# Optimization experiments

Hardware: AMD Instinct MI355X
Metric: run time of the kernel (lower is better)

Reference implementation:

```python
import jax, jax.numpy as jnp
import numpy as np
from jax import lax

B, S, H, T = 64, 512, 1024, 48


def setup_inputs() -> dict:
    key = jax.random.key(0)
    ks = jax.random.split(key, 8)
    x = jax.random.normal(ks[0], (B, S, H), dtype=jnp.float32)
    # left-aligned variable-length attention mask (lengths in [S//2, S])
    lengths = jax.random.randint(ks[1], (B,), S // 2, S + 1)
    attention_mask = (jnp.arange(S)[None, :] < lengths[:, None]).astype(jnp.int32)
    labels = jax.random.randint(ks[2], (B, S), 0, T).astype(jnp.int64)
    # decoder Linear(H, T)
    W = jax.random.normal(ks[3], (H, T), dtype=jnp.float32) / np.sqrt(H)
    b = jnp.zeros((T,), dtype=jnp.float32)
    # CRF parameters (allennlp-style: transitions + start/end transitions)
    transitions = jax.random.normal(ks[4], (T, T), dtype=jnp.float32) * 0.1
    start_trans = jax.random.normal(ks[5], (T,), dtype=jnp.float32) * 0.1
    end_trans = jax.random.normal(ks[6], (T,), dtype=jnp.float32) * 0.1
    return {"x": x, "attention_mask": attention_mask, "labels": labels,
            "W": W, "b": b, "transitions": transitions,
            "start_trans": start_trans, "end_trans": end_trans}


def _log_partition(logits, mask, trans, start, end):
    # logits [B,S,T], mask [B,S] int. Returns logZ [B].
    alpha0 = start[None, :] + logits[:, 0]                     # [B,T]
    emits = jnp.moveaxis(logits[:, 1:], 1, 0)                  # [S-1,B,T]
    ms = mask[:, 1:].T                                         # [S-1,B]

    def step(alpha, inp):
        emit, m = inp
        inner = alpha[:, :, None] + trans[None, :, :] + emit[:, None, :]  # [B,T,T]
        new = jax.nn.logsumexp(inner, axis=1)
        alpha = jnp.where(m[:, None] > 0, new, alpha)
        return alpha, None

    alpha, _ = lax.scan(step, alpha0, (emits, ms))
    return jax.nn.logsumexp(alpha + end[None, :], axis=1)      # [B]


def _gold_score(logits, labels, mask, trans, start, end):
    maskf = mask.astype(logits.dtype)
    emit = jnp.take_along_axis(logits, labels[..., None], axis=2)[..., 0]  # [B,S]
    emit_score = jnp.sum(emit * maskf, axis=1)
    tr = trans[labels[:, :-1], labels[:, 1:]]                   # [B,S-1]
    trans_score = jnp.sum(tr * maskf[:, 1:], axis=1)
    last_idx = jnp.sum(mask, axis=1) - 1                        # [B]
    last_tags = jnp.take_along_axis(labels, last_idx[:, None], axis=1)[:, 0]
    return start[labels[:, 0]] + emit_score + trans_score + end[last_tags]


def _viterbi(logits, mask, trans, start, end):
    Bn, Sn, Tn = logits.shape
    v0 = start[None, :] + logits[:, 0]
    emits = jnp.moveaxis(logits[:, 1:], 1, 0)                  # [S-1,B,T]
    ms = mask[:, 1:].T
    ident = jnp.broadcast_to(jnp.arange(Tn, dtype=jnp.int32)[None, :], (Bn, Tn))

    def step(v, inp):
        emit, m = inp
        scores = v[:, :, None] + trans[None, :, :]              # [B,T_prev,T_cur]
        bp = jnp.argmax(scores, axis=1).astype(jnp.int32)       # [B,T]
        best = jnp.max(scores, axis=1) + emit
        v_new = jnp.where(m[:, None] > 0, best, v)
        bp = jnp.where(m[:, None] > 0, bp, ident)               # identity at padded steps
        return v_new, bp

    v, bps = lax.scan(step, v0, (emits, ms))                    # bps [S-1,B,T]
    last = jnp.argmax(v + end[None, :], axis=1).astype(jnp.int32)  # [B]

    def back(tag, bp):
        prev = jnp.take_along_axis(bp, tag[:, None], axis=1)[:, 0]
        return prev, tag

    first_tag, rest = lax.scan(back, last, bps, reverse=True)   # rest [S-1,B]
    tags = jnp.concatenate([first_tag[:, None], rest.T], axis=1)  # [B,S]
    return (tags * mask).astype(jnp.int64)                      # pad with zeros


def reference(x, attention_mask, labels, W, b, transitions, start_trans, end_trans):
    features = jnp.einsum('bsh,ht->bst', x, W) + b              # decoder Linear
    pred_labels = _viterbi(features, attention_mask, transitions, start_trans, end_trans)
    logZ = _log_partition(features, attention_mask, transitions, start_trans, end_trans)
    gold = _gold_score(features, labels, attention_mask, transitions, start_trans, end_trans)
    loss = -jnp.sum(gold - logZ)                                # -log-likelihood, summed over batch
    return features, pred_labels, loss
```

## Files before the change

### kernel.cpp

```cpp
#include <hip/hip_runtime.h>
#include <hip/hip_bf16.h>
#include <math.h>

#define Bn 64
#define Sn 512
#define Hn 1024
#define Tn 48

#define LOG2E 1.4426950408889634f
#define LN2f  0.6931471805599453f

#define PRED_OFF (Bn*Sn*Tn)
#define LOSS_OFF (PRED_OFF + Bn*Sn)

#define RL(x,i) __int_as_float(__builtin_amdgcn_readlane(__float_as_int(x),(i)))

#if __has_builtin(__builtin_amdgcn_exp2f)
#define EXP2(x) __builtin_amdgcn_exp2f(x)
#else
#define EXP2(x) exp2f(x)
#endif
#if __has_builtin(__builtin_amdgcn_logf)
#define LOG2(x) __builtin_amdgcn_logf(x)
#else
#define LOG2(x) log2f(x)
#endif

__device__ __forceinline__ unsigned umin2(unsigned a, unsigned b) { return a < b ? a : b; }

#define DOT4(ACC,A,B) { ACC = fmaf((A).x,(B).x,ACC); ACC = fmaf((A).y,(B).y,ACC); ACC = fmaf((A).z,(B).z,ACC); ACC = fmaf((A).w,(B).w,ACC); }

__global__ __launch_bounds__(256) void gemm_feat(
    const float* __restrict__ x, const float* __restrict__ W,
    const float* __restrict__ bias, float* __restrict__ feat)
{
  __shared__ __align__(16) float xs[64][68];
  __shared__ __align__(16) float wsT[Tn][68];
  const int tid = threadIdx.x;
  const int srow = tid >> 2;
  const int sqc  = tid & 3;
  const int ty = tid >> 3;
  const int tx = tid & 7;
  const size_t row0 = (size_t)blockIdx.x * 64;

  float4 xreg[4];
  float  wreg[12];
  #pragma unroll
  for (int p = 0; p < 4; ++p)
    xreg[p] = *reinterpret_cast<const float4*>(&x[(row0 + srow)*Hn + (sqc + p*4)*4]);
  #pragma unroll
  for (int i = 0; i < 12; ++i) {
    const int id = tid + i*256; const int kk = id/Tn; const int t = id - kk*Tn;
    wreg[i] = W[(size_t)kk*Tn + t];
  }

  float acc[2][6];
  #pragma unroll
  for (int r = 0; r < 2; ++r)
    #pragma unroll
    for (int c = 0; c < 6; ++c) acc[r][c] = 0.f;

  for (int k0 = 0; k0 < Hn; k0 += 64) {
    #pragma unroll
    for (int p = 0; p < 4; ++p)
      *reinterpret_cast<float4*>(&xs[srow][(sqc + p*4)*4]) = xreg[p];
    #pragma unroll
    for (int i = 0; i < 12; ++i) {
      const int id = tid + i*256; const int kk = id/Tn; const int t = id - kk*Tn;
      wsT[t][kk] = wreg[i];
    }
    __syncthreads();
    if (k0 + 64 < Hn) {
      #pragma unroll
      for (int p = 0; p < 4; ++p)
        xreg[p] = *reinterpret_cast<const float4*>(&x[(row0 + srow)*Hn + (k0+64) + (sqc + p*4)*4]);
      #pragma unroll
      for (int i = 0; i < 12; ++i) {
        const int id = tid + i*256; const int kk = id/Tn; const int t = id - kk*Tn;
        wreg[i] = W[(size_t)(k0 + 64 + kk)*Tn + t];
      }
    }
    #pragma unroll 4
    for (int kk = 0; kk < 64; kk += 4) {
      const float4 a0 = *reinterpret_cast<const float4*>(&xs[ty*2+0][kk]);
      const float4 a1 = *reinterpret_cast<const float4*>(&xs[ty*2+1][kk]);
      const float4 w0 = *reinterpret_cast<const float4*>(&wsT[tx*6+0][kk]);
      const float4 w1 = *reinterpret_cast<const float4*>(&wsT[tx*6+1][kk]);
      const float4 w2 = *reinterpret_cast<const float4*>(&wsT[tx*6+2][kk]);
      const float4 w3 = *reinterpret_cast<const float4*>(&wsT[tx*6+3][kk]);
      const float4 w4 = *reinterpret_cast<const float4*>(&wsT[tx*6+4][kk]);
      const float4 w5 = *reinterpret_cast<const float4*>(&wsT[tx*6+5][kk]);
      DOT4(acc[0][0],a0,w0) DOT4(acc[0][1],a0,w1) DOT4(acc[0][2],a0,w2)
      DOT4(acc[0][3],a0,w3) DOT4(acc[0][4],a0,w4) DOT4(acc[0][5],a0,w5)
      DOT4(acc[1][0],a1,w0) DOT4(acc[1][1],a1,w1) DOT4(acc[1][2],a1,w2)
      DOT4(acc[1][3],a1,w3) DOT4(acc[1][4],a1,w4) DOT4(acc[1][5],a1,w5)
    }
    __syncthreads();
  }
  #pragma unroll
  for (int c = 0; c < 6; ++c) {
    const int col = tx*6 + c;
    const float bv = bias[col];
    #pragma unroll
    for (int r = 0; r < 2; ++r)
      feat[(row0 + ty*2 + r)*Tn + col] = acc[r][c] + bv;
  }
}

__global__ __launch_bounds__(64, 1) void crf_kernel(
    const float* __restrict__ feat,
    const int* __restrict__ mask,
    const int* __restrict__ labels,
    const float* __restrict__ trans,
    const float* __restrict__ startv,
    const float* __restrict__ endv,
    float* __restrict__ pred_out,
    float* __restrict__ wsLogZ,
    float* __restrict__ wsGold)
{
  __shared__ unsigned char bpL[Sn * 64];
  __shared__ unsigned char pathL[384 * 64];
  __shared__ __align__(16) float slds[64];
  __shared__ int EA[8];

  const int role = blockIdx.x >> 6;
  const int b    = blockIdx.x & 63;
  const int lane = threadIdx.x;
  const float* fb = feat + (size_t)b * Sn * Tn;

  int lc = 0;
  #pragma unroll
  for (int it = 0; it < Sn/64; ++it) lc += (mask[(size_t)b*Sn + it*64 + lane] != 0);
  #pragma unroll
  for (int off = 32; off; off >>= 1) lc += __shfl_xor(lc, off);
  const int len = lc;

  const int j = (lane < Tn) ? lane : (Tn - 1);
  const float4* sv4 = reinterpret_cast<const float4*>(slds);

  if (role == 0) {
    float Ev[48];
    #pragma unroll
    for (int i = 0; i < 48; ++i) Ev[i] = EXP2(trans[i*Tn + j] * LOG2E);
    const float a0 = (startv[j] + fb[j]) * LOG2E;
    float Zref = RL(a0, 0);
    float beta = a0 - Zref;
    slds[lane] = EXP2(beta);
    float em2 = fb[Tn + j] * LOG2E;
    for (int t = 1; t < len; ++t) {
      const int tn = (t + 1 < len) ? (t + 1) : t;
      const float em_nxt = fb[(size_t)tn*Tn + j] * LOG2E;
      float4 av[12];
      #pragma unroll
      for (int k = 0; k < 12; ++k) av[k] = sv4[k];
      float s0=0.f, s1=0.f, s2=0.f, s3=0.f;
      #pragma unroll
      for (int k = 0; k < 12; ++k) {
        s0 = fmaf(av[k].x, Ev[4*k+0], s0);
        s1 = fmaf(av[k].y, Ev[4*k+1], s1);
        s2 = fmaf(av[k].z, Ev[4*k+2], s2);
        s3 = fmaf(av[k].w, Ev[4*k+3], s3);
      }
      const float dj = LOG2((s0 + s1) + (s2 + s3)) + em2;
      const float d0 = RL(dj, 0);
      Zref += d0;
      const float nb = dj - d0;
      slds[lane] = EXP2(nb);
      beta = nb;
      em2 = em_nxt;
    }
    float fv = (lane < Tn) ? beta + endv[lane] * LOG2E : -INFINITY;
    float m = fv;
    #pragma unroll
    for (int off = 32; off; off >>= 1) m = fmaxf(m, __shfl_xor(m, off));
    float e = (lane < Tn) ? EXP2(fv - m) : 0.f;
    #pragma unroll
    for (int off = 32; off; off >>= 1) e += __shfl_xor(e, off);
    if (lane == 0) wsLogZ[b] = (Zref + m + LOG2(e)) * LN2f;

  } else if (role == 1) {
    float trv[48];
    #pragma unroll
    for (int i = 0; i < 48; ++i) trv[i] = trans[i*Tn + j];
    float v = startv[j] + fb[j];
    slds[lane] = v;
    float em_cur = fb[Tn + j];
    for (int t = 1; t < len; ++t) {
      const int tn = (t + 1 < len) ? (t + 1) : t;
      const float em_nxt = fb[(size_t)tn*Tn + j];
      float4 av[12];
      #pragma unroll
      for (int k = 0; k < 12; ++k) av[k] = sv4[k];
      float q[48];
      #pragma unroll
      for (int k = 0; k < 12; ++k) {
        q[4*k+0] = av[k].x + trv[4*k+0];
        q[4*k+1] = av[k].y + trv[4*k+1];
        q[4*k+2] = av[k].z + trv[4*k+2];
        q[4*k+3] = av[k].w + trv[4*k+3];
      }
      float m16[16];
      #pragma unroll
      for (int u = 0; u < 16; ++u)
        m16[u] = fmaxf(fmaxf(q[3*u], q[3*u+1]), q[3*u+2]);
      float m6a = fmaxf(fmaxf(m16[0],  m16[1]),  m16[2]);
      float m6b = fmaxf(fmaxf(m16[3],  m16[4]),  m16[5]);
      float m6c = fmaxf(fmaxf(m16[6],  m16[7]),  m16[8]);
      float m6d = fmaxf(fmaxf(m16[9],  m16[10]), m16[11]);
      float m6e = fmaxf(fmaxf(m16[12], m16[13]), m16[14]);
      float m6f = m16[15];
      const float best = fmaxf(fmaxf(fmaxf(m6a,m6b),m6c),
                               fmaxf(fmaxf(m6d,m6e),m6f));
      unsigned s16[16];
      #pragma unroll
      for (int u = 0; u < 16; ++u) {
        const unsigned ka = __float_as_uint(q[3*u]   - best) | (unsigned)(3*u);
        const unsigned kb = __float_as_uint(q[3*u+1] - best) | (unsigned)(3*u+1);
        const unsigned kc = __float_as_uint(q[3*u+2] - best) | (unsigned)(3*u+2);
        s16[u] = umin2(umin2(ka, kb), kc);
      }
      unsigned i6a = umin2(umin2(s16[0],  s16[1]),  s16[2]);
      unsigned i6b = umin2(umin2(s16[3],  s16[4]),  s16[5]);
      unsigned i6c = umin2(umin2(s16[6],  s16[7]),  s16[8]);
      unsigned i6d = umin2(umin2(s16[9],  s16[10]), s16[11]);
      unsigned i6e = umin2(umin2(s16[12], s16[13]), s16[14]);
      unsigned i6f = s16[15];
      const unsigned bidx = umin2(umin2(umin2(i6a,i6b),i6c), umin2(umin2(i6d,i6e),i6f));
      bpL[t*64 + lane] = (unsigned char)bidx;
      v = best + em_cur;
      slds[lane] = v;
      em_cur = em_nxt;
    }
    for (int t = len; t < Sn; ++t) bpL[t*64 + lane] = (unsigned char)lane;

    float fv = (lane < Tn) ? v + endv[lane] : -INFINITY;
    int fi = (lane < Tn) ? lane : 64;
    #pragma unroll
    for (int off = 32; off; off >>= 1) {
      const float ov = __shfl_xor(fv, off);
      const int   oi = __shfl_xor(fi, off);
      if (ov > fv || (ov == fv && oi < fi)) { fv = ov; fi = oi; }
    }
    __syncthreads();

    #define JOB(r) \
      const int id##r  = lane + 64*(r); \
      const int seg##r = id##r & 7;     \
      int cur##r = id##r >> 3;          \
      const int bpb##r = seg##r << 12;  \
      const int pb##r  = id##r << 6;    \
      pathL[pb##r + 63] = (unsigned char)cur##r;
    JOB(0) JOB(1) JOB(2) JOB(3) JOB(4) JOB(5)
    for (int d = 62; d >= 0; --d) {
      const int o = (d + 1) << 6;
      cur0 = bpL[bpb0 + o + cur0]; pathL[pb0 + d] = (unsigned char)cur0;
      cur1 = bpL[bpb1 + o + cur1]; pathL[pb1 + d] = (unsigned char)cur1;
      cur2 = bpL[bpb2 + o + cur2]; pathL[pb2 + d] = (unsigned char)cur2;
      cur3 = bpL[bpb3 + o + cur3]; pathL[pb3 + d] = (unsigned char)cur3;
      cur4 = bpL[bpb4 + o + cur4]; pathL[pb4 + d] = (unsigned char)cur4;
      cur5 = bpL[bpb5 + o + cur5]; pathL[pb5 + d] = (unsigned char)cur5;
    }
    #undef JOB
    __syncthreads();
    if (lane == 0) {
      int Ecur = fi;
      EA[7] = Ecur;
      for (int s = 7; s >= 1; --s) {
        const int bottom = pathL[((Ecur << 3) + s) * 64];
        Ecur = bpL[(s << 12) + bottom];
        EA[s-1] = Ecur;
      }
    }
    __syncthreads();
    #pragma unroll
    for (int r8 = 0; r8 < 8; ++r8) {
      const int t = r8*64 + lane;
      const int pv = pathL[((EA[r8] << 3) + r8) * 64 + lane];
      pred_out[(size_t)b*Sn + t] = (t < len) ? (float)pv : 0.f;
    }

  } else {
    float g = 0.f;
    #pragma unroll
    for (int it = 0; it < Sn/64; ++it) {
      const int sg = it*64 + lane;
      if (sg < len) {
        const int la = labels[(size_t)b*Sn + sg];
        float e = fb[(size_t)sg*Tn + la];
        if (sg > 0) e += trans[labels[(size_t)b*Sn + sg - 1]*Tn + la];
        g += e;
      }
    }
    #pragma unroll
    for (int off = 32; off; off >>= 1) g += __shfl_xor(g, off);
    if (lane == 0) {
      g += startv[labels[(size_t)b*Sn]] + endv[labels[(size_t)b*Sn + len - 1]];
      wsGold[b] = g;
    }
  }
}

__global__ void loss_reduce(const float* __restrict__ wsLogZ,
                            const float* __restrict__ wsGold,
                            float* __restrict__ out)
{
  const int lane = threadIdx.x;
  float v = wsLogZ[lane] - wsGold[lane];
  #pragma unroll
  for (int off = 32; off; off >>= 1) v += __shfl_xor(v, off);
  if (lane == 0) out[0] = v;
}

extern "C" void kernel_launch(void* const* d_in, const int* in_sizes, int n_in,
                              void* d_out, int out_size, void* d_ws, size_t ws_size,
                              hipStream_t stream) {
  const float* x      = (const float*)d_in[0];
  const int*   mask   = (const int*)  d_in[1];
  const int*   labels = (const int*)  d_in[2];
  const float* W      = (const float*)d_in[3];
  const float* bias   = (const float*)d_in[4];
  const float* trans  = (const float*)d_in[5];
  const float* startv = (const float*)d_in[6];
  const float* endv   = (const float*)d_in[7];

  float* out  = (float*)d_out;
  float* feat = out;
  float* pred = out + PRED_OFF;
  float* loss = out + LOSS_OFF;
  float* wsLogZ = (float*)d_ws;
  float* wsGold = wsLogZ + 64;

  gemm_feat<<<(Bn*Sn)/64, 256, 0, stream>>>(x, W, bias, feat);
  crf_kernel<<<192, 64, 0, stream>>>(feat, mask, labels, trans, startv, endv, pred, wsLogZ, wsGold);
  loss_reduce<<<1, 64, 0, stream>>>(wsLogZ, wsGold, loss);
}
```

Baseline: 323.9 us.

## Split Viterbi into serial max-scan, parallel backpointer pass, and backtrace kernel

```diff
diff --git a/kernel.cpp b/kernel.cpp
--- a/kernel.cpp
+++ b/kernel.cpp
@@ -27,6 +27,10 @@
 #endif
 
 __device__ __forceinline__ unsigned umin2(unsigned a, unsigned b) { return a < b ? a : b; }
+
+#define VWS_BYTE_OFF 512
+#define BPW_BYTE_OFF (512 + (size_t)Bn*Sn*Tn*4)
+#define WS_NEED (BPW_BYTE_OFF + (size_t)Bn*Sn*Tn)
 
 #define DOT4(ACC,A,B) { ACC = fmaf((A).x,(B).x,ACC); ACC = fmaf((A).y,(B).y,ACC); ACC = fmaf((A).z,(B).z,ACC); ACC = fmaf((A).w,(B).w,ACC); }
 
@@ -107,7 +111,284 @@
   }
 }
 
-__global__ __launch_bounds__(64, 1) void crf_kernel(
+__device__ __forceinline__ int seq_len(const int* __restrict__ mask, int b, int lane) {
+  int lc = 0;
+  #pragma unroll
+  for (int it = 0; it < Sn/64; ++it) lc += (mask[(size_t)b*Sn + it*64 + lane] != 0);
+  #pragma unroll
+  for (int off = 32; off; off >>= 1) lc += __shfl_xor(lc, off);
+  return lc;
+}
+
+__global__ __launch_bounds__(64, 1) void crf_scan(
+    const float* __restrict__ feat,
+    const int* __restrict__ mask,
+    const int* __restrict__ labels,
+    const float* __restrict__ trans,
+    const float* __restrict__ startv,
+    const float* __restrict__ endv,
+    float* __restrict__ vws,
+    float* __restrict__ wsLogZ,
+    float* __restrict__ wsGold)
+{
+  const int role = blockIdx.x >> 6;
+  const int b    = blockIdx.x & 63;
+  const int lane = threadIdx.x;
+  const float* fb = feat + (size_t)b * Sn * Tn;
+  const int len = seq_len(mask, b, lane);
+  const int j = (lane < Tn) ? lane : (Tn - 1);
+
+  if (role == 0) {
+    float Ev[48];
+    #pragma unroll
+    for (int i = 0; i < 48; ++i) Ev[i] = EXP2(trans[i*Tn + j] * LOG2E);
+    float emq[8];
+    #pragma unroll
+    for (int d = 0; d < 8; ++d) {
+      int s = 1 + d; s = s < len ? s : len - 1;
+      emq[d] = fb[(size_t)s * Tn + j];
+    }
+    const float a0 = (startv[j] + fb[j]) * LOG2E;
+    float Zref = RL(a0, 0);
+    float beta = a0 - Zref;
+    float p = EXP2(beta);
+    for (int t = 1; t < len; t += 8) {
+      #pragma unroll
+      for (int u = 0; u < 8; ++u) {
+        const int tt = t + u;
+        if (tt < len) {
+          const float em2 = emq[u] * LOG2E;
+          int tf = tt + 8; tf = tf < len ? tf : len - 1;
+          emq[u] = fb[(size_t)tf * Tn + j];
+          float s0=0.f, s1=0.f, s2=0.f, s3=0.f;
+          #pragma unroll
+          for (int k = 0; k < 12; ++k) {
+            s0 = fmaf(RL(p, 4*k+0), Ev[4*k+0], s0);
+            s1 = fmaf(RL(p, 4*k+1), Ev[4*k+1], s1);
+            s2 = fmaf(RL(p, 4*k+2), Ev[4*k+2], s2);
+            s3 = fmaf(RL(p, 4*k+3), Ev[4*k+3], s3);
+          }
+          const float dj = LOG2((s0 + s1) + (s2 + s3)) + em2;
+          const float d0 = RL(dj, 0);
+          Zref += d0;
+          beta = dj - d0;
+          p = EXP2(beta);
+        }
+      }
+    }
+    float fv = (lane < Tn) ? beta + endv[lane] * LOG2E : -INFINITY;
+    float m = fv;
+    #pragma unroll
+    for (int off = 32; off; off >>= 1) m = fmaxf(m, __shfl_xor(m, off));
+    float e = (lane < Tn) ? EXP2(fv - m) : 0.f;
+    #pragma unroll
+    for (int off = 32; off; off >>= 1) e += __shfl_xor(e, off);
+    if (lane == 0) wsLogZ[b] = (Zref + m + LOG2(e)) * LN2f;
+
+  } else if (role == 1) {
+    float trv[48];
+    #pragma unroll
+    for (int i = 0; i < 48; ++i) trv[i] = trans[i*Tn + j];
+    float emq[8];
+    #pragma unroll
+    for (int d = 0; d < 8; ++d) {
+      int s = 1 + d; s = s < len ? s : len - 1;
+      emq[d] = fb[(size_t)s * Tn + j];
+    }
+    float v = startv[j] + fb[j];
+    if (lane < Tn) vws[(size_t)b*Sn*Tn + lane] = v;
+    for (int t = 1; t < len; t += 8) {
+      #pragma unroll
+      for (int u = 0; u < 8; ++u) {
+        const int tt = t + u;
+        if (tt < len) {
+          const float em_cur = emq[u];
+          int tf = tt + 8; tf = tf < len ? tf : len - 1;
+          emq[u] = fb[(size_t)tf * Tn + j];
+          float q[48];
+          #pragma unroll
+          for (int i = 0; i < 48; ++i) q[i] = RL(v, i) + trv[i];
+          float m16[16];
+          #pragma unroll
+          for (int uu = 0; uu < 16; ++uu)
+            m16[uu] = fmaxf(fmaxf(q[3*uu], q[3*uu+1]), q[3*uu+2]);
+          float m6a = fmaxf(fmaxf(m16[0],  m16[1]),  m16[2]);
+          float m6b = fmaxf(fmaxf(m16[3],  m16[4]),  m16[5]);
+          float m6c = fmaxf(fmaxf(m16[6],  m16[7]),  m16[8]);
+          float m6d = fmaxf(fmaxf(m16[9],  m16[10]), m16[11]);
+          float m6e = fmaxf(fmaxf(m16[12], m16[13]), m16[14]);
+          const float best = fmaxf(fmaxf(fmaxf(m6a,m6b),m6c),
+                                   fmaxf(fmaxf(m6d,m6e),m16[15]));
+          v = best + em_cur;
+          if (lane < Tn) vws[((size_t)b*Sn + tt)*Tn + lane] = v;
+        }
+      }
+    }
+
+  } else {
+    float g = 0.f;
+    #pragma unroll
+    for (int it = 0; it < Sn/64; ++it) {
+      const int sg = it*64 + lane;
+      if (sg < len) {
+        const int la = labels[(size_t)b*Sn + sg];
+        float e = fb[(size_t)sg*Tn + la];
+        if (sg > 0) e += trans[labels[(size_t)b*Sn + sg - 1]*Tn + la];
+        g += e;
+      }
+    }
+    #pragma unroll
+    for (int off = 32; off; off >>= 1) g += __shfl_xor(g, off);
+    if (lane == 0) {
+      g += startv[labels[(size_t)b*Sn]] + endv[labels[(size_t)b*Sn + len - 1]];
+      wsGold[b] = g;
+    }
+  }
+}
+
+__global__ __launch_bounds__(256) void bp_kernel(
+    const float* __restrict__ vws,
+    const int* __restrict__ mask,
+    const float* __restrict__ trans,
+    unsigned char* __restrict__ bpw)
+{
+  const int b    = blockIdx.x >> 3;
+  const int oct  = blockIdx.x & 7;
+  const int wv   = threadIdx.x >> 6;
+  const int lane = threadIdx.x & 63;
+  const int len = seq_len(mask, b, lane);
+  const int j = (lane < Tn) ? lane : (Tn - 1);
+
+  float trv[48];
+  #pragma unroll
+  for (int i = 0; i < 48; ++i) trv[i] = trans[i*Tn + j];
+
+  const int t0 = oct*64 + wv*16;
+  #pragma unroll 2
+  for (int i = 0; i < 16; ++i) {
+    const int t = t0 + i;
+    int te = t; te = te < 1 ? 1 : te; te = te < len ? te : len - 1;
+    const float4* vp = reinterpret_cast<const float4*>(vws + ((size_t)b*Sn + te - 1)*Tn);
+    float q[48];
+    #pragma unroll
+    for (int k = 0; k < 12; ++k) {
+      const float4 a = vp[k];
+      q[4*k+0] = a.x + trv[4*k+0];
+      q[4*k+1] = a.y + trv[4*k+1];
+      q[4*k+2] = a.z + trv[4*k+2];
+      q[4*k+3] = a.w + trv[4*k+3];
+    }
+    float m16[16];
+    #pragma unroll
+    for (int u = 0; u < 16; ++u)
+      m16[u] = fmaxf(fmaxf(q[3*u], q[3*u+1]), q[3*u+2]);
+    float m6a = fmaxf(fmaxf(m16[0],  m16[1]),  m16[2]);
+    float m6b = fmaxf(fmaxf(m16[3],  m16[4]),  m16[5]);
+    float m6c = fmaxf(fmaxf(m16[6],  m16[7]),  m16[8]);
+    float m6d = fmaxf(fmaxf(m16[9],  m16[10]), m16[11]);
+    float m6e = fmaxf(fmaxf(m16[12], m16[13]), m16[14]);
+    const float best = fmaxf(fmaxf(fmaxf(m6a,m6b),m6c),
+                             fmaxf(fmaxf(m6d,m6e),m16[15]));
+    unsigned s16[16];
+    #pragma unroll
+    for (int u = 0; u < 16; ++u) {
+      const unsigned ka = __float_as_uint(q[3*u]   - best) | (unsigned)(3*u);
+      const unsigned kb = __float_as_uint(q[3*u+1] - best) | (unsigned)(3*u+1);
+      const unsigned kc = __float_as_uint(q[3*u+2] - best) | (unsigned)(3*u+2);
+      s16[u] = umin2(umin2(ka, kb), kc);
+    }
+    unsigned i6a = umin2(umin2(s16[0],  s16[1]),  s16[2]);
+    unsigned i6b = umin2(umin2(s16[3],  s16[4]),  s16[5]);
+    unsigned i6c = umin2(umin2(s16[6],  s16[7]),  s16[8]);
+    unsigned i6d = umin2(umin2(s16[9],  s16[10]), s16[11]);
+    unsigned i6e = umin2(umin2(s16[12], s16[13]), s16[14]);
+    const unsigned bidx = umin2(umin2(umin2(i6a,i6b),i6c), umin2(umin2(i6d,i6e),s16[15]));
+    if (t >= 1 && t < len && lane < Tn)
+      bpw[((size_t)b*Sn + t)*Tn + lane] = (unsigned char)bidx;
+  }
+}
+
+__device__ __forceinline__ unsigned idw(int a) {
+  return (unsigned)a | ((unsigned)(a+1)<<8) | ((unsigned)(a+2)<<16) | ((unsigned)(a+3)<<24);
+}
+
+__global__ __launch_bounds__(64, 1) void backtrace_kernel(
+    const float* __restrict__ vws,
+    const unsigned char* __restrict__ bpw,
+    const int* __restrict__ mask,
+    const float* __restrict__ endv,
+    float* __restrict__ pred_out)
+{
+  __shared__ unsigned char bpL[Sn * Tn];
+  __shared__ unsigned char pathL[384 * 64];
+  __shared__ int EA[8];
+
+  const int b    = blockIdx.x;
+  const int lane = threadIdx.x;
+  const int len = seq_len(mask, b, lane);
+
+  {
+    const uint4* gb = reinterpret_cast<const uint4*>(bpw + (size_t)b*Sn*Tn);
+    uint4* bl = reinterpret_cast<uint4*>(bpL);
+    for (int i4 = lane; i4 < Sn*Tn/16; i4 += 64) {
+      const int byte0 = i4*16;
+      const int t = byte0 / Tn;
+      const int j0 = byte0 - t*Tn;
+      uint4 val;
+      if (t >= 1 && t < len) val = gb[i4];
+      else { val.x = idw(j0); val.y = idw(j0+4); val.z = idw(j0+8); val.w = idw(j0+12); }
+      bl[i4] = val;
+    }
+  }
+
+  float fv = (lane < Tn) ? vws[((size_t)b*Sn + len - 1)*Tn + lane] + endv[lane] : -INFINITY;
+  int fi = (lane < Tn) ? lane : 64;
+  #pragma unroll
+  for (int off = 32; off; off >>= 1) {
+    const float ov = __shfl_xor(fv, off);
+    const int   oi = __shfl_xor(fi, off);
+    if (ov > fv || (ov == fv && oi < fi)) { fv = ov; fi = oi; }
+  }
+  __syncthreads();
+
+  #define JOB(r) \
+    const int id##r  = lane + 64*(r); \
+    const int seg##r = id##r & 7;     \
+    int cur##r = id##r >> 3;          \
+    const int bpb##r = seg##r * 64 * Tn; \
+    const int pb##r  = id##r << 6;    \
+    pathL[pb##r + 63] = (unsigned char)cur##r;
+  JOB(0) JOB(1) JOB(2) JOB(3) JOB(4) JOB(5)
+  for (int d = 62; d >= 0; --d) {
+    const int o = (d + 1) * Tn;
+    cur0 = bpL[bpb0 + o + cur0]; pathL[pb0 + d] = (unsigned char)cur0;
+    cur1 = bpL[bpb1 + o + cur1]; pathL[pb1 + d] = (unsigned char)cur1;
+    cur2 = bpL[bpb2 + o + cur2]; pathL[pb2 + d] = (unsigned char)cur2;
+    cur3 = bpL[bpb3 + o + cur3]; pathL[pb3 + d] = (unsigned char)cur3;
+    cur4 = bpL[bpb4 + o + cur4]; pathL[pb4 + d] = (unsigned char)cur4;
+    cur5 = bpL[bpb5 + o + cur5]; pathL[pb5 + d] = (unsigned char)cur5;
+  }
+  #undef JOB
+  __syncthreads();
+  if (lane == 0) {
+    int Ecur = fi;
+    EA[7] = Ecur;
+    for (int s = 7; s >= 1; --s) {
+      const int bottom = pathL[((Ecur << 3) + s) * 64];
+      Ecur = bpL[(s * 64) * Tn + bottom];
+      EA[s-1] = Ecur;
+    }
+  }
+  __syncthreads();
+  #pragma unroll
+  for (int r8 = 0; r8 < 8; ++r8) {
+    const int t = r8*64 + lane;
+    const int pv = pathL[((EA[r8] << 3) + r8) * 64 + lane];
+    pred_out[(size_t)b*Sn + t] = (t < len) ? (float)pv : 0.f;
+  }
+}
+
+__global__ __launch_bounds__(64, 1) void crf_kernel_fb(
     const float* __restrict__ feat,
     const int* __restrict__ mask,
     const int* __restrict__ labels,
@@ -127,14 +408,7 @@
   const int b    = blockIdx.x & 63;
   const int lane = threadIdx.x;
   const float* fb = feat + (size_t)b * Sn * Tn;
-
-  int lc = 0;
-  #pragma unroll
-  for (int it = 0; it < Sn/64; ++it) lc += (mask[(size_t)b*Sn + it*64 + lane] != 0);
-  #pragma unroll
-  for (int off = 32; off; off >>= 1) lc += __shfl_xor(lc, off);
-  const int len = lc;
-
+  const int len = seq_len(mask, b, lane);
   const int j = (lane < Tn) ? lane : (Tn - 1);
   const float4* sv4 = reinterpret_cast<const float4*>(slds);
 
@@ -201,38 +475,35 @@
       }
       float m16[16];
       #pragma unroll
-      for (int u = 0; u < 16; ++u)
-        m16[u] = fmaxf(fmaxf(q[3*u], q[3*u+1]), q[3*u+2]);
+      for (int uu = 0; uu < 16; ++uu)
+        m16[uu] = fmaxf(fmaxf(q[3*uu], q[3*uu+1]), q[3*uu+2]);
       float m6a = fmaxf(fmaxf(m16[0],  m16[1]),  m16[2]);
       float m6b = fmaxf(fmaxf(m16[3],  m16[4]),  m16[5]);
       float m6c = fmaxf(fmaxf(m16[6],  m16[7]),  m16[8]);
       float m6d = fmaxf(fmaxf(m16[9],  m16[10]), m16[11]);
       float m6e = fmaxf(fmaxf(m16[12], m16[13]), m16[14]);
-      float m6f = m16[15];
       const float best = fmaxf(fmaxf(fmaxf(m6a,m6b),m6c),
-                               fmaxf(fmaxf(m6d,m6e),m6f));
+                               fmaxf(fmaxf(m6d,m6e),m16[15]));
+      v = best + em_cur;
+      slds[lane] = v;
       unsigned s16[16];
       #pragma unroll
-      for (int u = 0; u < 16; ++u) {
-        const unsigned ka = __float_as_uint(q[3*u]   - best) | (unsigned)(3*u);
-        const unsigned kb = __float_as_uint(q[3*u+1] - best) | (unsigned)(3*u+1);
-        const unsigned kc = __float_as_uint(q[3*u+2] - best) | (unsigned)(3*u+2);
-        s16[u] = umin2(umin2(ka, kb), kc);
+      for (int uu = 0; uu < 16; ++uu) {
+        const unsigned ka = __float_as_uint(q[3*uu]   - best) | (unsigned)(3*uu);
+        const unsigned kb = __float_as_uint(q[3*uu+1] - best) | (unsigned)(3*uu+1);
+        const unsigned kc = __float_as_uint(q[3*uu+2] - best) | (unsigned)(3*uu+2);
+        s16[uu] = umin2(umin2(ka, kb), kc);
       }
       unsigned i6a = umin2(umin2(s16[0],  s16[1]),  s16[2]);
       unsigned i6b = umin2(umin2(s16[3],  s16[4]),  s16[5]);
       unsigned i6c = umin2(umin2(s16[6],  s16[7]),  s16[8]);
       unsigned i6d = umin2(umin2(s16[9],  s16[10]), s16[11]);
       unsigned i6e = umin2(umin2(s16[12], s16[13]), s16[14]);
-      unsigned i6f = s16[15];
-      const unsigned bidx = umin2(umin2(umin2(i6a,i6b),i6c), umin2(umin2(i6d,i6e),i6f));
+      const unsigned bidx = umin2(umin2(umin2(i6a,i6b),i6c), umin2(umin2(i6d,i6e),s16[15]));
       bpL[t*64 + lane] = (unsigned char)bidx;
-      v = best + em_cur;
-      slds[lane] = v;
       em_cur = em_nxt;
     }
     for (int t = len; t < Sn; ++t) bpL[t*64 + lane] = (unsigned char)lane;
-
     float fv = (lane < Tn) ? v + endv[lane] : -INFINITY;
     int fi = (lane < Tn) ? lane : 64;
     #pragma unroll
@@ -242,15 +513,14 @@
       if (ov > fv || (ov == fv && oi < fi)) { fv = ov; fi = oi; }
     }
     __syncthreads();
-
-    #define JOB(r) \
+    #define JOBF(r) \
       const int id##r  = lane + 64*(r); \
       const int seg##r = id##r & 7;     \
       int cur##r = id##r >> 3;          \
       const int bpb##r = seg##r << 12;  \
       const int pb##r  = id##r << 6;    \
       pathL[pb##r + 63] = (unsigned char)cur##r;
-    JOB(0) JOB(1) JOB(2) JOB(3) JOB(4) JOB(5)
+    JOBF(0) JOBF(1) JOBF(2) JOBF(3) JOBF(4) JOBF(5)
     for (int d = 62; d >= 0; --d) {
       const int o = (d + 1) << 6;
       cur0 = bpL[bpb0 + o + cur0]; pathL[pb0 + d] = (unsigned char)cur0;
@@ -260,7 +530,7 @@
       cur4 = bpL[bpb4 + o + cur4]; pathL[pb4 + d] = (unsigned char)cur4;
       cur5 = bpL[bpb5 + o + cur5]; pathL[pb5 + d] = (unsigned char)cur5;
     }
-    #undef JOB
+    #undef JOBF
     __syncthreads();
     if (lane == 0) {
       int Ecur = fi;
@@ -278,7 +548,6 @@
       const int pv = pathL[((EA[r8] << 3) + r8) * 64 + lane];
       pred_out[(size_t)b*Sn + t] = (t < len) ? (float)pv : 0.f;
     }
-
   } else {
     float g = 0.f;
     #pragma unroll
@@ -331,6 +600,15 @@
   float* wsGold = wsLogZ + 64;
 
   gemm_feat<<<(Bn*Sn)/64, 256, 0, stream>>>(x, W, bias, feat);
-  crf_kernel<<<192, 64, 0, stream>>>(feat, mask, labels, trans, startv, endv, pred, wsLogZ, wsGold);
+
+  if (ws_size >= WS_NEED) {
+    float* vws = (float*)((char*)d_ws + VWS_BYTE_OFF);
+    unsigned char* bpw = (unsigned char*)d_ws + BPW_BYTE_OFF;
+    crf_scan<<<192, 64, 0, stream>>>(feat, mask, labels, trans, startv, endv, vws, wsLogZ, wsGold);
+    bp_kernel<<<512, 256, 0, stream>>>(vws, mask, trans, bpw);
+    backtrace_kernel<<<64, 64, 0, stream>>>(vws, bpw, mask, endv, pred);
+  } else {
+    crf_kernel_fb<<<192, 64, 0, stream>>>(feat, mask, labels, trans, startv, endv, pred, wsLogZ, wsGold);
+  }
   loss_reduce<<<1, 64, 0, stream>>>(wsLogZ, wsGold, loss);
 }
```

Result: slower. 366.9 us (+13.3%).

## Move Viterbi backpointer argmax off the serial scan into a parallel kernel

Applied to the files above, without the earlier changes.

```diff
diff --git a/kernel.cpp b/kernel.cpp
--- a/kernel.cpp
+++ b/kernel.cpp
@@ -26,7 +26,12 @@
 #define LOG2(x) log2f(x)
 #endif
 
+#define PIN(x) asm volatile("" : "+v"(x))
+
 __device__ __forceinline__ unsigned umin2(unsigned a, unsigned b) { return a < b ? a : b; }
+
+#define VWS_BYTE_OFF 512
+#define BPW_BYTE_OFF (512 + (size_t)Bn*Sn*Tn*4)
 
 #define DOT4(ACC,A,B) { ACC = fmaf((A).x,(B).x,ACC); ACC = fmaf((A).y,(B).y,ACC); ACC = fmaf((A).z,(B).z,ACC); ACC = fmaf((A).w,(B).w,ACC); }
 
@@ -34,36 +39,36 @@
     const float* __restrict__ x, const float* __restrict__ W,
     const float* __restrict__ bias, float* __restrict__ feat)
 {
-  __shared__ __align__(16) float xs[64][68];
+  __shared__ __align__(16) float xs[128][68];
   __shared__ __align__(16) float wsT[Tn][68];
   const int tid = threadIdx.x;
-  const int srow = tid >> 2;
-  const int sqc  = tid & 3;
+  const int srow  = tid >> 1;
+  const int shalf = tid & 1;
   const int ty = tid >> 3;
   const int tx = tid & 7;
-  const size_t row0 = (size_t)blockIdx.x * 64;
-
-  float4 xreg[4];
+  const size_t row0 = (size_t)blockIdx.x * 128;
+
+  float4 xreg[8];
   float  wreg[12];
   #pragma unroll
-  for (int p = 0; p < 4; ++p)
-    xreg[p] = *reinterpret_cast<const float4*>(&x[(row0 + srow)*Hn + (sqc + p*4)*4]);
+  for (int p = 0; p < 8; ++p)
+    xreg[p] = *reinterpret_cast<const float4*>(&x[(row0 + srow)*Hn + shalf*32 + p*4]);
   #pragma unroll
   for (int i = 0; i < 12; ++i) {
     const int id = tid + i*256; const int kk = id/Tn; const int t = id - kk*Tn;
     wreg[i] = W[(size_t)kk*Tn + t];
   }
 
-  float acc[2][6];
-  #pragma unroll
-  for (int r = 0; r < 2; ++r)
+  float acc[4][6];
+  #pragma unroll
+  for (int r = 0; r < 4; ++r)
     #pragma unroll
     for (int c = 0; c < 6; ++c) acc[r][c] = 0.f;
 
   for (int k0 = 0; k0 < Hn; k0 += 64) {
     #pragma unroll
-    for (int p = 0; p < 4; ++p)
-      *reinterpret_cast<float4*>(&xs[srow][(sqc + p*4)*4]) = xreg[p];
+    for (int p = 0; p < 8; ++p)
+      *reinterpret_cast<float4*>(&xs[srow][shalf*32 + p*4]) = xreg[p];
     #pragma unroll
     for (int i = 0; i < 12; ++i) {
       const int id = tid + i*256; const int kk = id/Tn; const int t = id - kk*Tn;
@@ -72,8 +77,8 @@
     __syncthreads();
     if (k0 + 64 < Hn) {
       #pragma unroll
-      for (int p = 0; p < 4; ++p)
-        xreg[p] = *reinterpret_cast<const float4*>(&x[(row0 + srow)*Hn + (k0+64) + (sqc + p*4)*4]);
+      for (int p = 0; p < 8; ++p)
+        xreg[p] = *reinterpret_cast<const float4*>(&x[(row0 + srow)*Hn + (k0+64) + shalf*32 + p*4]);
       #pragma unroll
       for (int i = 0; i < 12; ++i) {
         const int id = tid + i*256; const int kk = id/Tn; const int t = id - kk*Tn;
@@ -82,8 +87,10 @@
     }
     #pragma unroll 4
     for (int kk = 0; kk < 64; kk += 4) {
-      const float4 a0 = *reinterpret_cast<const float4*>(&xs[ty*2+0][kk]);
-      const float4 a1 = *reinterpret_cast<const float4*>(&xs[ty*2+1][kk]);
+      const float4 a0 = *reinterpret_cast<const float4*>(&xs[ty*4+0][kk]);
+      const float4 a1 = *reinterpret_cast<const float4*>(&xs[ty*4+1][kk]);
+      const float4 a2 = *reinterpret_cast<const float4*>(&xs[ty*4+2][kk]);
+      const float4 a3 = *reinterpret_cast<const float4*>(&xs[ty*4+3][kk]);
       const float4 w0 = *reinterpret_cast<const float4*>(&wsT[tx*6+0][kk]);
       const float4 w1 = *reinterpret_cast<const float4*>(&wsT[tx*6+1][kk]);
       const float4 w2 = *reinterpret_cast<const float4*>(&wsT[tx*6+2][kk]);
@@ -94,6 +101,10 @@
       DOT4(acc[0][3],a0,w3) DOT4(acc[0][4],a0,w4) DOT4(acc[0][5],a0,w5)
       DOT4(acc[1][0],a1,w0) DOT4(acc[1][1],a1,w1) DOT4(acc[1][2],a1,w2)
       DOT4(acc[1][3],a1,w3) DOT4(acc[1][4],a1,w4) DOT4(acc[1][5],a1,w5)
+      DOT4(acc[2][0],a2,w0) DOT4(acc[2][1],a2,w1) DOT4(acc[2][2],a2,w2)
+      DOT4(acc[2][3],a2,w3) DOT4(acc[2][4],a2,w4) DOT4(acc[2][5],a2,w5)
+      DOT4(acc[3][0],a3,w0) DOT4(acc[3][1],a3,w1) DOT4(acc[3][2],a3,w2)
+      DOT4(acc[3][3],a3,w3) DOT4(acc[3][4],a3,w4) DOT4(acc[3][5],a3,w5)
     }
     __syncthreads();
   }
@@ -102,72 +113,77 @@
     const int col = tx*6 + c;
     const float bv = bias[col];
     #pragma unroll
-    for (int r = 0; r < 2; ++r)
-      feat[(row0 + ty*2 + r)*Tn + col] = acc[r][c] + bv;
-  }
-}
-
-__global__ __launch_bounds__(64, 1) void crf_kernel(
+    for (int r = 0; r < 4; ++r)
+      feat[(row0 + ty*4 + r)*Tn + col] = acc[r][c] + bv;
+  }
+}
+
+__device__ __forceinline__ int seq_len(const int* __restrict__ mask, int b, int lane) {
+  int lc = 0;
+  #pragma unroll
+  for (int it = 0; it < Sn/64; ++it) lc += (mask[(size_t)b*Sn + it*64 + lane] != 0);
+  #pragma unroll
+  for (int off = 32; off; off >>= 1) lc += __shfl_xor(lc, off);
+  return lc;
+}
+
+__global__ __launch_bounds__(64, 1) void crf_scan(
     const float* __restrict__ feat,
     const int* __restrict__ mask,
     const int* __restrict__ labels,
     const float* __restrict__ trans,
     const float* __restrict__ startv,
     const float* __restrict__ endv,
-    float* __restrict__ pred_out,
+    float* __restrict__ vws,
     float* __restrict__ wsLogZ,
     float* __restrict__ wsGold)
 {
-  __shared__ unsigned char bpL[Sn * 64];
-  __shared__ unsigned char pathL[384 * 64];
-  __shared__ __align__(16) float slds[64];
-  __shared__ int EA[8];
-
   const int role = blockIdx.x >> 6;
   const int b    = blockIdx.x & 63;
   const int lane = threadIdx.x;
   const float* fb = feat + (size_t)b * Sn * Tn;
-
-  int lc = 0;
-  #pragma unroll
-  for (int it = 0; it < Sn/64; ++it) lc += (mask[(size_t)b*Sn + it*64 + lane] != 0);
-  #pragma unroll
-  for (int off = 32; off; off >>= 1) lc += __shfl_xor(lc, off);
-  const int len = lc;
-
+  const int len = seq_len(mask, b, lane);
   const int j = (lane < Tn) ? lane : (Tn - 1);
-  const float4* sv4 = reinterpret_cast<const float4*>(slds);
 
   if (role == 0) {
     float Ev[48];
     #pragma unroll
     for (int i = 0; i < 48; ++i) Ev[i] = EXP2(trans[i*Tn + j] * LOG2E);
+    #pragma unroll
+    for (int i = 0; i < 48; ++i) PIN(Ev[i]);
+    float emq[8];
+    #pragma unroll
+    for (int d = 0; d < 8; ++d) {
+      int s = 1 + d; s = s < len ? s : len - 1;
+      emq[d] = fb[(size_t)s * Tn + j];
+    }
     const float a0 = (startv[j] + fb[j]) * LOG2E;
     float Zref = RL(a0, 0);
     float beta = a0 - Zref;
-    slds[lane] = EXP2(beta);
-    float em2 = fb[Tn + j] * LOG2E;
-    for (int t = 1; t < len; ++t) {
-      const int tn = (t + 1 < len) ? (t + 1) : t;
-      const float em_nxt = fb[(size_t)tn*Tn + j] * LOG2E;
-      float4 av[12];
+    float p = EXP2(beta);
+    for (int t = 1; t < len; t += 8) {
       #pragma unroll
-      for (int k = 0; k < 12; ++k) av[k] = sv4[k];
-      float s0=0.f, s1=0.f, s2=0.f, s3=0.f;
-      #pragma unroll
-      for (int k = 0; k < 12; ++k) {
-        s0 = fmaf(av[k].x, Ev[4*k+0], s0);
-        s1 = fmaf(av[k].y, Ev[4*k+1], s1);
-        s2 = fmaf(av[k].z, Ev[4*k+2], s2);
-        s3 = fmaf(av[k].w, Ev[4*k+3], s3);
+      for (int u = 0; u < 8; ++u) {
+        const int tt = t + u;
+        if (tt < len) {
+          const float em2 = emq[u] * LOG2E;
+          int tf = tt + 8; tf = tf < len ? tf : len - 1;
+          emq[u] = fb[(size_t)tf * Tn + j];
+          float s0=0.f, s1=0.f, s2=0.f, s3=0.f;
+          #pragma unroll
+          for (int k = 0; k < 12; ++k) {
+            s0 = fmaf(RL(p, 4*k+0), Ev[4*k+0], s0);
+            s1 = fmaf(RL(p, 4*k+1), Ev[4*k+1], s1);
+            s2 = fmaf(RL(p, 4*k+2), Ev[4*k+2], s2);
+            s3 = fmaf(RL(p, 4*k+3), Ev[4*k+3], s3);
+          }
+          const float dj = LOG2((s0 + s1) + (s2 + s3)) + em2;
+          const float d0 = RL(dj, 0);
+          Zref += d0;
+          beta = dj - d0;
+          p = EXP2(beta);
+        }
       }
-      const float dj = LOG2((s0 + s1) + (s2 + s3)) + em2;
-      const float d0 = RL(dj, 0);
-      Zref += d0;
-      const float nb = dj - d0;
-      slds[lane] = EXP2(nb);
-      beta = nb;
-      em2 = em_nxt;
     }
     float fv = (lane < Tn) ? beta + endv[lane] * LOG2E : -INFINITY;
     float m = fv;
@@ -182,101 +198,42 @@
     float trv[48];
     #pragma unroll
     for (int i = 0; i < 48; ++i) trv[i] = trans[i*Tn + j];
+    #pragma unroll
+    for (int i = 0; i < 48; ++i) PIN(trv[i]);
+    float emq[8];
+    #pragma unroll
+    for (int d = 0; d < 8; ++d) {
+      int s = 1 + d; s = s < len ? s : len - 1;
+      emq[d] = fb[(size_t)s * Tn + j];
+    }
     float v = startv[j] + fb[j];
-    slds[lane] = v;
-    float em_cur = fb[Tn + j];
-    for (int t = 1; t < len; ++t) {
-      const int tn = (t + 1 < len) ? (t + 1) : t;
-      const float em_nxt = fb[(size_t)tn*Tn + j];
-      float4 av[12];
+    if (lane < Tn) vws[(size_t)b*Sn*Tn + lane] = v;
+    for (int t = 1; t < len; t += 8) {
       #pragma unroll
-      for (int k = 0; k < 12; ++k) av[k] = sv4[k];
-      float q[48];
-      #pragma unroll
-      for (int k = 0; k < 12; ++k) {
-        q[4*k+0] = av[k].x + trv[4*k+0];
-        q[4*k+1] = av[k].y + trv[4*k+1];
-        q[4*k+2] = av[k].z + trv[4*k+2];
-        q[4*k+3] = av[k].w + trv[4*k+3];
+      for (int u = 0; u < 8; ++u) {
+        const int tt = t + u;
+        if (tt < len) {
+          const float em_cur = emq[u];
+          int tf = tt + 8; tf = tf < len ? tf : len - 1;
+          emq[u] = fb[(size_t)tf * Tn + j];
+          float q[48];
+          #pragma unroll
+          for (int i = 0; i < 48; ++i) q[i] = RL(v, i) + trv[i];
+          float m16[16];
+          #pragma unroll
+          for (int uu = 0; uu < 16; ++uu)
+            m16[uu] = fmaxf(fmaxf(q[3*uu], q[3*uu+1]), q[3*uu+2]);
+          float m6a = fmaxf(fmaxf(m16[0],  m16[1]),  m16[2]);
+          float m6b = fmaxf(fmaxf(m16[3],  m16[4]),  m16[5]);
+          float m6c = fmaxf(fmaxf(m16[6],  m16[7]),  m16[8]);
+          float m6d = fmaxf(fmaxf(m16[9],  m16[10]), m16[11]);
+          float m6e = fmaxf(fmaxf(m16[12], m16[13]), m16[14]);
+          const float best = fmaxf(fmaxf(fmaxf(m6a,m6b),m6c),
+                                   fmaxf(fmaxf(m6d,m6e),m16[15]));
+          v = best + em_cur;
+          if (lane < Tn) vws[((size_t)b*Sn + tt)*Tn + lane] = v;
+        }
       }
-      float m16[16];
-      #pragma unroll
-      for (int u = 0; u < 16; ++u)
-        m16[u] = fmaxf(fmaxf(q[3*u], q[3*u+1]), q[3*u+2]);
-      float m6a = fmaxf(fmaxf(m16[0],  m16[1]),  m16[2]);
-      float m6b = fmaxf(fmaxf(m16[3],  m16[4]),  m16[5]);
-      float m6c = fmaxf(fmaxf(m16[6],  m16[7]),  m16[8]);
-      float m6d = fmaxf(fmaxf(m16[9],  m16[10]), m16[11]);
-      float m6e = fmaxf(fmaxf(m16[12], m16[13]), m16[14]);
-      float m6f = m16[15];
-      const float best = fmaxf(fmaxf(fmaxf(m6a,m6b),m6c),
-                               fmaxf(fmaxf(m6d,m6e),m6f));
-      unsigned s16[16];
-      #pragma unroll
-      for (int u = 0; u < 16; ++u) {
-        const unsigned ka = __float_as_uint(q[3*u]   - best) | (unsigned)(3*u);
-        const unsigned kb = __float_as_uint(q[3*u+1] - best) | (unsigned)(3*u+1);
-        const unsigned kc = __float_as_uint(q[3*u+2] - best) | (unsigned)(3*u+2);
-        s16[u] = umin2(umin2(ka, kb), kc);
-      }
-      unsigned i6a = umin2(umin2(s16[0],  s16[1]),  s16[2]);
-      unsigned i6b = umin2(umin2(s16[3],  s16[4]),  s16[5]);
-      unsigned i6c = umin2(umin2(s16[6],  s16[7]),  s16[8]);
-      unsigned i6d = umin2(umin2(s16[9],  s16[10]), s16[11]);
-      unsigned i6e = umin2(umin2(s16[12], s16[13]), s16[14]);
-      unsigned i6f = s16[15];
-      const unsigned bidx = umin2(umin2(umin2(i6a,i6b),i6c), umin2(umin2(i6d,i6e),i6f));
-      bpL[t*64 + lane] = (unsigned char)bidx;
-      v = best + em_cur;
-      slds[lane] = v;
-      em_cur = em_nxt;
-    }
-    for (int t = len; t < Sn; ++t) bpL[t*64 + lane] = (unsigned char)lane;
-
-    float fv = (lane < Tn) ? v + endv[lane] : -INFINITY;
-    int fi = (lane < Tn) ? lane : 64;
-    #pragma unroll
-    for (int off = 32; off; off >>= 1) {
-      const float ov = __shfl_xor(fv, off);
-      const int   oi = __shfl_xor(fi, off);
-      if (ov > fv || (ov == fv && oi < fi)) { fv = ov; fi = oi; }
-    }
-    __syncthreads();
-
-    #define JOB(r) \
-      const int id##r  = lane + 64*(r); \
-      const int seg##r = id##r & 7;     \
-      int cur##r = id##r >> 3;          \
-      const int bpb##r = seg##r << 12;  \
-      const int pb##r  = id##r << 6;    \
-      pathL[pb##r + 63] = (unsigned char)cur##r;
-    JOB(0) JOB(1) JOB(2) JOB(3) JOB(4) JOB(5)
-    for (int d = 62; d >= 0; --d) {
-      const int o = (d + 1) << 6;
-      cur0 = bpL[bpb0 + o + cur0]; pathL[pb0 + d] = (unsigned char)cur0;
-      cur1 = bpL[bpb1 + o + cur1]; pathL[pb1 + d] = (unsigned char)cur1;
-      cur2 = bpL[bpb2 + o + cur2]; pathL[pb2 + d] = (unsigned char)cur2;
-      cur3 = bpL[bpb3 + o + cur3]; pathL[pb3 + d] = (unsigned char)cur3;
-      cur4 = bpL[bpb4 + o + cur4]; pathL[pb4 + d] = (unsigned char)cur4;
-      cur5 = bpL[bpb5 + o + cur5]; pathL[pb5 + d] = (unsigned char)cur5;
-    }
-    #undef JOB
-    __syncthreads();
-    if (lane == 0) {
-      int Ecur = fi;
-      EA[7] = Ecur;
-      for (int s = 7; s >= 1; --s) {
-        const int bottom = pathL[((Ecur << 3) + s) * 64];
-        Ecur = bpL[(s << 12) + bottom];
-        EA[s-1] = Ecur;
-      }
-    }
-    __syncthreads();
-    #pragma unroll
-    for (int r8 = 0; r8 < 8; ++r8) {
-      const int t = r8*64 + lane;
-      const int pv = pathL[((EA[r8] << 3) + r8) * 64 + lane];
-      pred_out[(size_t)b*Sn + t] = (t < len) ? (float)pv : 0.f;
     }
 
   } else {
@@ -297,6 +254,150 @@
       g += startv[labels[(size_t)b*Sn]] + endv[labels[(size_t)b*Sn + len - 1]];
       wsGold[b] = g;
     }
+  }
+}
+
+__global__ __launch_bounds__(256) void bp_kernel(
+    const float* __restrict__ vws,
+    const int* __restrict__ mask,
+    const float* __restrict__ trans,
+    unsigned char* __restrict__ bpw)
+{
+  const int b    = blockIdx.x >> 3;
+  const int oct  = blockIdx.x & 7;
+  const int wv   = threadIdx.x >> 6;
+  const int lane = threadIdx.x & 63;
+  const int len = seq_len(mask, b, lane);
+  const int j = (lane < Tn) ? lane : (Tn - 1);
+
+  float trv[48];
+  #pragma unroll
+  for (int i = 0; i < 48; ++i) trv[i] = trans[i*Tn + j];
+  #pragma unroll
+  for (int i = 0; i < 48; ++i) PIN(trv[i]);
+
+  const int t0 = oct*64 + wv*16;
+  #pragma unroll 2
+  for (int i = 0; i < 16; ++i) {
+    const int t = t0 + i;
+    int te = t; te = te < 1 ? 1 : te; te = te < len ? te : len - 1;
+    const float4* vp = reinterpret_cast<const float4*>(vws + ((size_t)b*Sn + te - 1)*Tn);
+    float q[48];
+    #pragma unroll
+    for (int k = 0; k < 12; ++k) {
+      const float4 a = vp[k];
+      q[4*k+0] = a.x + trv[4*k+0];
+      q[4*k+1] = a.y + trv[4*k+1];
+      q[4*k+2] = a.z + trv[4*k+2];
+      q[4*k+3] = a.w + trv[4*k+3];
+    }
+    float m16[16];
+    #pragma unroll
+    for (int u = 0; u < 16; ++u)
+      m16[u] = fmaxf(fmaxf(q[3*u], q[3*u+1]), q[3*u+2]);
+    float m6a = fmaxf(fmaxf(m16[0],  m16[1]),  m16[2]);
+    float m6b = fmaxf(fmaxf(m16[3],  m16[4]),  m16[5]);
+    float m6c = fmaxf(fmaxf(m16[6],  m16[7]),  m16[8]);
+    float m6d = fmaxf(fmaxf(m16[9],  m16[10]), m16[11]);
+    float m6e = fmaxf(fmaxf(m16[12], m16[13]), m16[14]);
+    const float best = fmaxf(fmaxf(fmaxf(m6a,m6b),m6c),
+                             fmaxf(fmaxf(m6d,m6e),m16[15]));
+    unsigned s16[16];
+    #pragma unroll
+    for (int u = 0; u < 16; ++u) {
+      const unsigned ka = __float_as_uint(q[3*u]   - best) | (unsigned)(3*u);
+      const unsigned kb = __float_as_uint(q[3*u+1] - best) | (unsigned)(3*u+1);
+      const unsigned kc = __float_as_uint(q[3*u+2] - best) | (unsigned)(3*u+2);
+      s16[u] = umin2(umin2(ka, kb), kc);
+    }
+    unsigned i6a = umin2(umin2(s16[0],  s16[1]),  s16[2]);
+    unsigned i6b = umin2(umin2(s16[3],  s16[4]),  s16[5]);
+    unsigned i6c = umin2(umin2(s16[6],  s16[7]),  s16[8]);
+    unsigned i6d = umin2(umin2(s16[9],  s16[10]), s16[11]);
+    unsigned i6e = umin2(umin2(s16[12], s16[13]), s16[14]);
+    const unsigned bidx = umin2(umin2(umin2(i6a,i6b),i6c), umin2(umin2(i6d,i6e),s16[15]));
+    if (t >= 1 && t < len && lane < Tn)
+      bpw[((size_t)b*Sn + t)*Tn + lane] = (unsigned char)bidx;
+  }
+}
+
+__device__ __forceinline__ unsigned idw(int a) {
+  return (unsigned)a | ((unsigned)(a+1)<<8) | ((unsigned)(a+2)<<16) | ((unsigned)(a+3)<<24);
+}
+
+__global__ __launch_bounds__(64, 1) void backtrace_kernel(
+    const float* __restrict__ vws,
+    const unsigned char* __restrict__ bpw,
+    const int* __restrict__ mask,
+    const float* __restrict__ endv,
+    float* __restrict__ pred_out)
+{
+  __shared__ unsigned char bpL[Sn * Tn];
+  __shared__ unsigned char pathL[384 * 64];
+  __shared__ int EA[8];
+
+  const int b    = blockIdx.x;
+  const int lane = threadIdx.x;
+  const int len = seq_len(mask, b, lane);
+
+  {
+    const uint4* gb = reinterpret_cast<const uint4*>(bpw + (size_t)b*Sn*Tn);
+    uint4* bl = reinterpret_cast<uint4*>(bpL);
+    for (int i4 = lane; i4 < Sn*Tn/16; i4 += 64) {
+      const int byte0 = i4*16;
+      const int t = byte0 / Tn;
+      const int j0 = byte0 - t*Tn;
+      uint4 val;
+      if (t >= 1 && t < len) val = gb[i4];
+      else { val.x = idw(j0); val.y = idw(j0+4); val.z = idw(j0+8); val.w = idw(j0+12); }
+      bl[i4] = val;
+    }
+  }
+
+  float fv = (lane < Tn) ? vws[((size_t)b*Sn + len - 1)*Tn + lane] + endv[lane] : -INFINITY;
+  int fi = (lane < Tn) ? lane : 64;
+  #pragma unroll
+  for (int off = 32; off; off >>= 1) {
+    const float ov = __shfl_xor(fv, off);
+    const int   oi = __shfl_xor(fi, off);
+    if (ov > fv || (ov == fv && oi < fi)) { fv = ov; fi = oi; }
+  }
+  __syncthreads();
+
+  #define JOB(r) \
+    const int id##r  = lane + 64*(r); \
+    const int seg##r = id##r & 7;     \
+    int cur##r = id##r >> 3;          \
+    const int bpb##r = seg##r * 64 * Tn; \
+    const int pb##r  = id##r << 6;    \
+    pathL[pb##r + 63] = (unsigned char)cur##r;
+  JOB(0) JOB(1) JOB(2) JOB(3) JOB(4) JOB(5)
+  for (int d = 62; d >= 0; --d) {
+    const int o = (d + 1) * Tn;
+    cur0 = bpL[bpb0 + o + cur0]; pathL[pb0 + d] = (unsigned char)cur0;
+    cur1 = bpL[bpb1 + o + cur1]; pathL[pb1 + d] = (unsigned char)cur1;
+    cur2 = bpL[bpb2 + o + cur2]; pathL[pb2 + d] = (unsigned char)cur2;
+    cur3 = bpL[bpb3 + o + cur3]; pathL[pb3 + d] = (unsigned char)cur3;
+    cur4 = bpL[bpb4 + o + cur4]; pathL[pb4 + d] = (unsigned char)cur4;
+    cur5 = bpL[bpb5 + o + cur5]; pathL[pb5 + d] = (unsigned char)cur5;
+  }
+  #undef JOB
+  __syncthreads();
+  if (lane == 0) {
+    int Ecur = fi;
+    EA[7] = Ecur;
+    for (int s = 7; s >= 1; --s) {
+      const int bottom = pathL[((Ecur << 3) + s) * 64];
+      Ecur = bpL[(s * 64) * Tn + bottom];
+      EA[s-1] = Ecur;
+    }
+  }
+  __syncthreads();
+  #pragma unroll
+  for (int r8 = 0; r8 < 8; ++r8) {
+    const int t = r8*64 + lane;
+    const int pv = pathL[((EA[r8] << 3) + r8) * 64 + lane];
+    pred_out[(size_t)b*Sn + t] = (t < len) ? (float)pv : 0.f;
   }
 }
 
@@ -329,8 +430,12 @@
   float* loss = out + LOSS_OFF;
   float* wsLogZ = (float*)d_ws;
   float* wsGold = wsLogZ + 64;
-
-  gemm_feat<<<(Bn*Sn)/64, 256, 0, stream>>>(x, W, bias, feat);
-  crf_kernel<<<192, 64, 0, stream>>>(feat, mask, labels, trans, startv, endv, pred, wsLogZ, wsGold);
+  float* vws = (float*)((char*)d_ws + VWS_BYTE_OFF);
+  unsigned char* bpw = (unsigned char*)d_ws + BPW_BYTE_OFF;
+
+  gemm_feat<<<(Bn*Sn)/128, 256, 0, stream>>>(x, W, bias, feat);
+  crf_scan<<<192, 64, 0, stream>>>(feat, mask, labels, trans, startv, endv, vws, wsLogZ, wsGold);
+  bp_kernel<<<512, 256, 0, stream>>>(vws, mask, trans, bpw);
+  backtrace_kernel<<<64, 64, 0, stream>>>(vws, bpw, mask, endv, pred);
   loss_reduce<<<1, 64, 0, stream>>>(wsLogZ, wsGold, loss);
 }
```

Result: slower. 397.4 us (+22.7%).
